# Optimization experiments

Measured on AMD Instinct MI355X. Metric: run time of the kernel, lower is better.

Reference implementation:

```python
import jax, jax.numpy as jnp
import numpy as np

B, N, D = 2, 2048, 1024
H, ENC = 16, 8
HD = D // H
EPS = 1e-5


def _apply_rope(x, cos, sin):
    # x: [B,N,H,HD], cos/sin: [N,HD//2]
    c = cos[None, :, None, :]
    s = sin[None, :, None, :]
    x_re = x[..., 0::2]
    x_im = x[..., 1::2]
    out = jnp.stack([x_re * c - x_im * s, x_re * s + x_im * c], axis=-1)
    return out.reshape(x.shape)


def _rmsnorm(x):
    return x * jax.lax.rsqrt(jnp.mean(x * x, axis=-1, keepdims=True) + EPS)


def setup_inputs() -> dict:
    key = jax.random.key(0)
    ks = jax.random.split(key, 8)
    pos = jnp.arange(N, dtype=jnp.float32)[:, None]
    inv_freq = 1.0 / (10000.0 ** (jnp.arange(0, HD, 2, dtype=jnp.float32) / HD))  # [HD//2]
    ang = pos * inv_freq[None, :]
    std = 0.02
    return {
        "x": jax.random.normal(ks[0], (B, N, D), dtype=jnp.float32),
        "rope_cos": jnp.cos(ang),
        "rope_sin": jnp.sin(ang),
        "Wq": std * jax.random.normal(ks[1], (D, D), dtype=jnp.float32),
        "Wk": std * jax.random.normal(ks[2], (D, D), dtype=jnp.float32),
        "Wv": std * jax.random.normal(ks[3], (D, D), dtype=jnp.float32),
        "Wo_enc": std * jax.random.normal(ks[4], (H * HD, D), dtype=jnp.float32),
        "Wo_dec": std * jax.random.normal(ks[5], ((H - ENC) * HD, D), dtype=jnp.float32),
        "heads": H,
        "encoder_heads": ENC,
    }


def reference(x, rope_cos, rope_sin, Wq, Wk, Wv, Wo_enc, Wo_dec, heads, encoder_heads):
    b, n, d = x.shape
    hd = d // heads
    scale = hd ** (-0.5)
    q = (x @ Wq).reshape(b, n, heads, hd)
    k = (x @ Wk).reshape(b, n, heads, hd)
    v = (x @ Wv).reshape(b, n, heads, hd)
    q = _rmsnorm(_apply_rope(q, rope_cos, rope_sin))
    k = _rmsnorm(_apply_rope(k, rope_cos, rope_sin))
    # scores: [B,H,N,N]
    scores = jnp.einsum("bihd,bjhd->bhij", q, k) * scale
    causal = jnp.tril(jnp.ones((n, n), dtype=bool))  # [N,N]
    is_enc = (jnp.arange(heads) < encoder_heads)[:, None, None]  # [H,1,1]
    allow = jnp.logical_or(is_enc, causal[None, :, :])  # [H,N,N]
    scores = jnp.where(allow[None], scores, -jnp.inf)
    att = jax.nn.softmax(scores, axis=-1)
    out = jnp.einsum("bhij,bjhd->bihd", att, v)  # [B,N,H,HD]
    enc_out = out.reshape(b, n, heads * hd) @ Wo_enc
    dec_out = out[:, :, encoder_heads:, :].reshape(b, n, (heads - encoder_heads) * hd) @ Wo_dec
    return (enc_out, dec_out)
```

## Files before the change

### kernel.cpp

```cpp
#include <hip/hip_runtime.h>
#include <hip/hip_bf16.h>
#include <math.h>

#define B_    2
#define N_    2048
#define D_    1024
#define H_    16
#define ENC_  8
#define HD_   64
#define EPS_  1e-5f
#define M_    (B_ * N_)

typedef __bf16 bf16x8 __attribute__((ext_vector_type(8)));
typedef __bf16 bf16x2 __attribute__((ext_vector_type(2)));
typedef float  f32x4  __attribute__((ext_vector_type(4)));

#define MB(x) ((size_t)(x) * 1024 * 1024)

#define KSC_  0.18033688011112042f

#if __has_builtin(__builtin_amdgcn_exp2f)
#define EXP2F(x) __builtin_amdgcn_exp2f(x)
#else
#define EXP2F(x) exp2f(x)
#endif

__device__ __forceinline__ void gld16(const __bf16* g, __bf16* l) {
    __builtin_amdgcn_global_load_lds(
        (const __attribute__((address_space(1))) void*)g,
        (__attribute__((address_space(3))) void*)l,
        16, 0, 0);
}

template <typename OutT>
__device__ __forceinline__ void gemm_core(
    const __bf16* __restrict__ A, const __bf16* __restrict__ Bt,
    OutT* __restrict__ C, int K, int lda, int aoff, int ldc,
    int bm, int bn, __bf16* As, __bf16* Bs)
{
    const int tid  = threadIdx.x;
    const int w    = tid >> 6;
    const int lane = tid & 63;
    const int lrow = lane & 15;
    const int quad = lane >> 4;
    const int wr   = w >> 1;
    const int wc   = w & 1;

    const int sr = lane >> 3;
    const int cl = lane & 7;
    const int sk = ((cl ^ sr) * 8);

    const __bf16* Ag0 = A  + (size_t)(bm +  0 + w * 8 + sr) * lda + aoff + sk;
    const __bf16* Ag1 = A  + (size_t)(bm + 32 + w * 8 + sr) * lda + aoff + sk;
    const __bf16* Ag2 = A  + (size_t)(bm + 64 + w * 8 + sr) * lda + aoff + sk;
    const __bf16* Ag3 = A  + (size_t)(bm + 96 + w * 8 + sr) * lda + aoff + sk;
    const __bf16* Bg0 = Bt + (size_t)(bn +  0 + w * 8 + sr) * K + sk;
    const __bf16* Bg1 = Bt + (size_t)(bn + 32 + w * 8 + sr) * K + sk;
    const __bf16* Bg2 = Bt + (size_t)(bn + 64 + w * 8 + sr) * K + sk;
    const __bf16* Bg3 = Bt + (size_t)(bn + 96 + w * 8 + sr) * K + sk;

    f32x4 acc[4][4];
    #pragma unroll
    for (int i = 0; i < 4; ++i)
        #pragma unroll
        for (int j = 0; j < 4; ++j) acc[i][j] = (f32x4){0.f, 0.f, 0.f, 0.f};

    auto stage = [&](int k0, int bb) {
        __bf16* Al = As + bb * 8192 + w * 8 * 64;
        __bf16* Bl = Bs + bb * 8192 + w * 8 * 64;
        gld16(Ag0 + k0, Al);
        gld16(Ag1 + k0, Al + 2048);
        gld16(Ag2 + k0, Al + 4096);
        gld16(Ag3 + k0, Al + 6144);
        gld16(Bg0 + k0, Bl);
        gld16(Bg1 + k0, Bl + 2048);
        gld16(Bg2 + k0, Bl + 4096);
        gld16(Bg3 + k0, Bl + 6144);
    };

    stage(0, 0);
    __syncthreads();
    int bb = 0;
    for (int k0 = 0; k0 < K; k0 += 64, bb ^= 1) {
        if (k0 + 64 < K) stage(k0 + 64, bb ^ 1);
        const __bf16* Ab = As + bb * 8192;
        const __bf16* Bb = Bs + bb * 8192;
        #pragma unroll
        for (int h = 0; h < 2; ++h) {
            const int ch = ((h * 4 + quad) ^ (lrow & 7)) * 8;
            bf16x8 af[4], bf[4];
            #pragma unroll
            for (int rt = 0; rt < 4; ++rt)
                af[rt] = *(const bf16x8*)&Ab[(wr * 64 + rt * 16 + lrow) * 64 + ch];
            #pragma unroll
            for (int ct = 0; ct < 4; ++ct)
                bf[ct] = *(const bf16x8*)&Bb[(wc * 64 + ct * 16 + lrow) * 64 + ch];

            #pragma unroll
            for (int rt = 0; rt < 4; ++rt)
                #pragma unroll
                for (int ct = 0; ct < 4; ++ct)
                    acc[rt][ct] = __builtin_amdgcn_mfma_f32_16x16x32_bf16(
                        af[rt], bf[ct], acc[rt][ct], 0, 0, 0);
        }
        __syncthreads();
    }

    #pragma unroll
    for (int rt = 0; rt < 4; ++rt)
        #pragma unroll
        for (int ct = 0; ct < 4; ++ct)
            #pragma unroll
            for (int r = 0; r < 4; ++r) {
                const int row = bm + wr * 64 + rt * 16 + quad * 4 + r;
                const int col = bn + wc * 64 + ct * 16 + lrow;
                C[(size_t)row * ldc + col] = (OutT)acc[rt][ct][r];
            }
}

__global__ __launch_bounds__(256) void gemm_qkv(
    const __bf16* __restrict__ A, const __bf16* __restrict__ Bt,
    __bf16* __restrict__ C)
{
    __shared__ __bf16 As[2 * 128 * 64];
    __shared__ __bf16 Bs[2 * 128 * 64];
    gemm_core<__bf16>(A, Bt, C, D_, D_, 0, 3072,
                      blockIdx.y * 128, blockIdx.x * 128, As, Bs);
}

__global__ __launch_bounds__(256) void gemm_out(
    const __bf16* __restrict__ A, const __bf16* __restrict__ Woe,
    const __bf16* __restrict__ Wod, float* __restrict__ Cenc,
    float* __restrict__ Cdec)
{
    __shared__ __bf16 As[2 * 128 * 64];
    __shared__ __bf16 Bs[2 * 128 * 64];
    const int id = blockIdx.x;
    if (id < 256) {
        gemm_core<float>(A, Woe, Cenc, 1024, D_, 0, D_,
                         (id >> 3) * 128, (id & 7) * 128, As, Bs);
    } else {
        const int idx = id - 256;
        gemm_core<float>(A, Wod, Cdec, 512, D_, 512, D_,
                         (idx >> 3) * 128, (idx & 7) * 128, As, Bs);
    }
}

struct WtArgs {
    const float* W[5];
    __bf16*      Wt[5];
    int          K[5];
    int          nyb[5];
    const float* x;
    __bf16*      xbf;
};

__global__ __launch_bounds__(256) void wt_conv_all(WtArgs ar)
{
    const int z = blockIdx.z;
    if (z >= 5) {
        const int linear = (z - 5) * 256 + blockIdx.y * 16 + blockIdx.x;
        const size_t i = ((size_t)linear * 256 + threadIdx.x) * 8;
        float4 a = *(const float4*)&ar.x[i];
        float4 b = *(const float4*)&ar.x[i + 4];
        bf16x8 o = {(__bf16)a.x, (__bf16)a.y, (__bf16)a.z, (__bf16)a.w,
                    (__bf16)b.x, (__bf16)b.y, (__bf16)b.z, (__bf16)b.w};
        *(bf16x8*)&ar.xbf[i] = o;
        return;
    }
    if (blockIdx.y >= ar.nyb[z]) return;
    const float* W  = ar.W[z];
    __bf16*      Wt = ar.Wt[z];
    const int    K  = ar.K[z];

    __shared__ __bf16 t[64][72];
    const int kb = blockIdx.y * 64;
    const int nb = blockIdx.x * 64;
    {
        const int kl = threadIdx.x >> 2;
        const int c0 = (threadIdx.x & 3) * 16;
        const float* src = W + (size_t)(kb + kl) * D_ + nb + c0;
        #pragma unroll
        for (int u = 0; u < 4; ++u) {
            float4 f = *(const float4*)&src[u * 4];
            t[c0 + u * 4 + 0][kl] = (__bf16)f.x;
            t[c0 + u * 4 + 1][kl] = (__bf16)f.y;
            t[c0 + u * 4 + 2][kl] = (__bf16)f.z;
            t[c0 + u * 4 + 3][kl] = (__bf16)f.w;
        }
    }
    __syncthreads();
    {
        const int nl  = threadIdx.x >> 2;
        const int k0c = (threadIdx.x & 3) * 16;
        __bf16* dst = Wt + (size_t)(nb + nl) * K + kb + k0c;
        *(bf16x8*)&dst[0] = *(const bf16x8*)&t[nl][k0c];
        *(bf16x8*)&dst[8] = *(const bf16x8*)&t[nl][k0c + 8];
    }
}

__global__ __launch_bounds__(256) void rope_vconv(
    const __bf16* __restrict__ qkv,
    const float* __restrict__ cs, const float* __restrict__ sn,
    __bf16* __restrict__ qbf, __bf16* __restrict__ kbf,
    __bf16* __restrict__ vt)
{
    if (blockIdx.x < 16384) {
        const int row  = blockIdx.x * 4 + (threadIdx.x >> 6);
        const int lane = threadIdx.x & 63;
        const int n    = (row >> 4) & (N_ - 1);
        const int b    = row >> 15;
        const int h    = row & 15;
        const int p    = lane >> 1;

        const float c = cs[n * (HD_ / 2) + p];
        const float s = sn[n * (HD_ / 2) + p];
        const size_t ibase = (size_t)(b * N_ + n) * 3072 + h * HD_ + lane;
        const size_t obase = ((size_t)(b * H_ + h) * N_ + n) * HD_ + lane;
        const bool odd = (lane & 1);

        {
            float val = (float)qkv[ibase];
            float partner = __shfl_xor(val, 1, 64);
            float r = odd ? fmaf(partner, s, val * c)
                          : (val * c - partner * s);
            float ss = r * r;
            #pragma unroll
            for (int off = 1; off < 64; off <<= 1) ss += __shfl_xor(ss, off, 64);
            qbf[obase] = (__bf16)(r * rsqrtf(ss * (1.0f / 64.0f) + EPS_) * KSC_);
        }
        {
            float val = (float)qkv[ibase + 1024];
            float partner = __shfl_xor(val, 1, 64);
            float r = odd ? fmaf(partner, s, val * c)
                          : (val * c - partner * s);
            float ss = r * r;
            #pragma unroll
            for (int off = 1; off < 64; off <<= 1) ss += __shfl_xor(ss, off, 64);
            kbf[obase] = (__bf16)(r * rsqrtf(ss * (1.0f / 64.0f) + EPS_));
        }
    } else {
        __shared__ __bf16 tile[64][72];
        const int bx = blockIdx.x - 16384;
        const int bh = bx >> 5;
        const int b  = bh >> 4, h = bh & 15;
        const int n0 = (bx & 31) * 64;
        {
            const int nl = threadIdx.x >> 2;
            const int d0 = (threadIdx.x & 3) * 16;
            const __bf16* src =
                qkv + (size_t)(b * N_ + n0 + nl) * 3072 + 2048 + h * HD_ + d0;
            bf16x8 v0 = *(const bf16x8*)&src[0];
            bf16x8 v1 = *(const bf16x8*)&src[8];
            #pragma unroll
            for (int e = 0; e < 8; ++e) {
                tile[d0 + e][nl]     = v0[e];
                tile[d0 + 8 + e][nl] = v1[e];
            }
        }
        __syncthreads();
        {
            const int dl = threadIdx.x >> 2;
            const int nc = (threadIdx.x & 3) * 16;
            __bf16* dst = vt + ((size_t)(bh * HD_ + dl)) * N_ + n0 + nc;
            bf16x8 o0, o1;
            #pragma unroll
            for (int e = 0; e < 8; ++e) {
                const int p0 = nc + e;
                const int p1 = nc + 8 + e;
                o0[e] = tile[dl][(p0 & ~31) + (((p0 >> 2) & 1) << 4)
                                 + (((p0 >> 3) & 3) << 2) + (p0 & 3)];
                o1[e] = tile[dl][(p1 & ~31) + (((p1 >> 2) & 1) << 4)
                                 + (((p1 >> 3) & 3) << 2) + (p1 & 3)];
            }
            *(bf16x8*)&dst[0] = o0;
            *(bf16x8*)&dst[8] = o1;
        }
    }
}

template <int NG, bool DEC>
__device__ __forceinline__ void attn_core(
    const __bf16* __restrict__ qbase, const __bf16* __restrict__ kbase,
    const __bf16* __restrict__ vbase, __bf16* __restrict__ o,
    int b, int h, int qb, int ntiles,
    __bf16 (*Ks)[4096], __bf16 (*Vs)[4096])
{
    const int tid  = threadIdx.x;
    const int w    = tid >> 6;
    const int lane = tid & 63;
    const int lrow = lane & 15;
    const int quad = lane >> 4;

    const __bf16* kg0 = kbase + (size_t)lane * HD_ + w * 8;
    const __bf16* kg1 = kbase + (size_t)lane * HD_ + (w + 4) * 8;
    const __bf16* vg  = vbase + (size_t)lane * N_;

    int i0g[NG];
    #pragma unroll
    for (int g = 0; g < NG; ++g) i0g[g] = qb * (NG * 64) + g * 64 + w * 16;

    bf16x8 qf[NG][2];
    #pragma unroll
    for (int g = 0; g < NG; ++g)
        #pragma unroll
        for (int kc = 0; kc < 2; ++kc)
            qf[g][kc] = *(const bf16x8*)
                &qbase[(size_t)(i0g[g] + lrow) * HD_ + kc * 32 + quad * 8];

    const f32x4 zero = {0.f, 0.f, 0.f, 0.f};
    f32x4 oacc[NG][4];
    float lsum[NG];
    #pragma unroll
    for (int g = 0; g < NG; ++g) {
        lsum[g] = 0.f;
        #pragma unroll
        for (int c = 0; c < 4; ++c) oacc[g][c] = zero;
    }

    auto stage = [&](int t, int bb) {
        const int j0 = t << 6;
        gld16(kg0 + (size_t)j0 * HD_, &Ks[bb][(w)     * 512]);
        gld16(kg1 + (size_t)j0 * HD_, &Ks[bb][(w + 4) * 512]);
        gld16(vg + j0 + w * 8,        &Vs[bb][(w)     * 512]);
        gld16(vg + j0 + (w + 4) * 8,  &Vs[bb][(w + 4) * 512]);
    };

    stage(0, 0);
    for (int t = 0; t < ntiles; ++t) {
        const int bb = t & 1;
        __syncthreads();
        if (t + 1 < ntiles) stage(t + 1, bb ^ 1);

        const int j64 = t << 6;
        const bool do1 = !DEC || (j64 + 32 <= i0g[0] + 15);

        bf16x8 pf[2][NG];

        {
            bf16x8 kf0 = *(const bf16x8*)&Ks[bb][((quad)     * 64 + lrow) * 8];
            bf16x8 kf1 = *(const bf16x8*)&Ks[bb][((4 + quad) * 64 + lrow) * 8];
            bf16x8 kf2 = *(const bf16x8*)&Ks[bb][((quad)     * 64 + 16 + lrow) * 8];
            bf16x8 kf3 = *(const bf16x8*)&Ks[bb][((4 + quad) * 64 + 16 + lrow) * 8];

            f32x4 s0[NG], s1[NG];
            #pragma unroll
            for (int g = 0; g < NG; ++g) { s0[g] = zero; s1[g] = zero; }
            #pragma unroll
            for (int g = 0; g < NG; ++g)
                s0[g] = __builtin_amdgcn_mfma_f32_16x16x32_bf16(kf0, qf[g][0], s0[g], 0, 0, 0);
            #pragma unroll
            for (int g = 0; g < NG; ++g)
                s0[g] = __builtin_amdgcn_mfma_f32_16x16x32_bf16(kf1, qf[g][1], s0[g], 0, 0, 0);
            #pragma unroll
            for (int g = 0; g < NG; ++g)
                s1[g] = __builtin_amdgcn_mfma_f32_16x16x32_bf16(kf2, qf[g][0], s1[g], 0, 0, 0);
            #pragma unroll
            for (int g = 0; g < NG; ++g)
                s1[g] = __builtin_amdgcn_mfma_f32_16x16x32_bf16(kf3, qf[g][1], s1[g], 0, 0, 0);

            #pragma unroll
            for (int g = 0; g < NG; ++g) {
                float pA[4], pB[4];
                if (DEC && (j64 + 31 > i0g[g])) {
                    const int i = i0g[g] + lrow;
                    #pragma unroll
                    for (int r = 0; r < 4; ++r) {
                        const int k0 = j64 + quad * 4 + r;
                        pA[r] = (k0      <= i) ? EXP2F(s0[g][r]) : 0.f;
                        pB[r] = (k0 + 16 <= i) ? EXP2F(s1[g][r]) : 0.f;
                    }
                } else {
                    #pragma unroll
                    for (int r = 0; r < 4; ++r) {
                        pA[r] = EXP2F(s0[g][r]);
                        pB[r] = EXP2F(s1[g][r]);
                    }
                }
                lsum[g] += (pA[0] + pA[1]) + (pA[2] + pA[3])
                         + (pB[0] + pB[1]) + (pB[2] + pB[3]);
                pf[0][g] = (bf16x8){(__bf16)pA[0], (__bf16)pA[1],
                                    (__bf16)pA[2], (__bf16)pA[3],
                                    (__bf16)pB[0], (__bf16)pB[1],
                                    (__bf16)pB[2], (__bf16)pB[3]};
            }
        }

        if (do1) {
            bf16x8 kf0 = *(const bf16x8*)&Ks[bb][((quad)     * 64 + 32 + lrow) * 8];
            bf16x8 kf1 = *(const bf16x8*)&Ks[bb][((4 + quad) * 64 + 32 + lrow) * 8];
            bf16x8 kf2 = *(const bf16x8*)&Ks[bb][((quad)     * 64 + 48 + lrow) * 8];
            bf16x8 kf3 = *(const bf16x8*)&Ks[bb][((4 + quad) * 64 + 48 + lrow) * 8];

            f32x4 s0[NG], s1[NG];
            #pragma unroll
            for (int g = 0; g < NG; ++g) { s0[g] = zero; s1[g] = zero; }
            #pragma unroll
            for (int g = 0; g < NG; ++g)
                s0[g] = __builtin_amdgcn_mfma_f32_16x16x32_bf16(kf0, qf[g][0], s0[g], 0, 0, 0);
            #pragma unroll
            for (int g = 0; g < NG; ++g)
                s0[g] = __builtin_amdgcn_mfma_f32_16x16x32_bf16(kf1, qf[g][1], s0[g], 0, 0, 0);
            #pragma unroll
            for (int g = 0; g < NG; ++g)
                s1[g] = __builtin_amdgcn_mfma_f32_16x16x32_bf16(kf2, qf[g][0], s1[g], 0, 0, 0);
            #pragma unroll
            for (int g = 0; g < NG; ++g)
                s1[g] = __builtin_amdgcn_mfma_f32_16x16x32_bf16(kf3, qf[g][1], s1[g], 0, 0, 0);

            const int jp = j64 + 32;
            #pragma unroll
            for (int g = 0; g < NG; ++g) {
                float pA[4], pB[4];
                if (DEC && (jp + 31 > i0g[g])) {
                    const int i = i0g[g] + lrow;
                    #pragma unroll
                    for (int r = 0; r < 4; ++r) {
                        const int k0 = jp + quad * 4 + r;
                        pA[r] = (k0      <= i) ? EXP2F(s0[g][r]) : 0.f;
                        pB[r] = (k0 + 16 <= i) ? EXP2F(s1[g][r]) : 0.f;
                    }
                } else {
                    #pragma unroll
                    for (int r = 0; r < 4; ++r) {
                        pA[r] = EXP2F(s0[g][r]);
                        pB[r] = EXP2F(s1[g][r]);
                    }
                }
                lsum[g] += (pA[0] + pA[1]) + (pA[2] + pA[3])
                         + (pB[0] + pB[1]) + (pB[2] + pB[3]);
                pf[1][g] = (bf16x8){(__bf16)pA[0], (__bf16)pA[1],
                                    (__bf16)pA[2], (__bf16)pA[3],
                                    (__bf16)pB[0], (__bf16)pB[1],
                                    (__bf16)pB[2], (__bf16)pB[3]};
            }
        }

        {
            bf16x8 vf0 = *(const bf16x8*)&Vs[bb][((quad) * 64 +  0 + lrow) * 8];
            bf16x8 vf1 = *(const bf16x8*)&Vs[bb][((quad) * 64 + 16 + lrow) * 8];
            bf16x8 vf2 = *(const bf16x8*)&Vs[bb][((quad) * 64 + 32 + lrow) * 8];
            bf16x8 vf3 = *(const bf16x8*)&Vs[bb][((quad) * 64 + 48 + lrow) * 8];
            #pragma unroll
            for (int g = 0; g < NG; ++g) {
                oacc[g][0] = __builtin_amdgcn_mfma_f32_16x16x32_bf16(pf[0][g], vf0, oacc[g][0], 0, 0, 0);
                oacc[g][1] = __builtin_amdgcn_mfma_f32_16x16x32_bf16(pf[0][g], vf1, oacc[g][1], 0, 0, 0);
                oacc[g][2] = __builtin_amdgcn_mfma_f32_16x16x32_bf16(pf[0][g], vf2, oacc[g][2], 0, 0, 0);
                oacc[g][3] = __builtin_amdgcn_mfma_f32_16x16x32_bf16(pf[0][g], vf3, oacc[g][3], 0, 0, 0);
            }
        }

        if (do1) {
            bf16x8 vf0 = *(const bf16x8*)&Vs[bb][((4 + quad) * 64 +  0 + lrow) * 8];
            bf16x8 vf1 = *(const bf16x8*)&Vs[bb][((4 + quad) * 64 + 16 + lrow) * 8];
            bf16x8 vf2 = *(const bf16x8*)&Vs[bb][((4 + quad) * 64 + 32 + lrow) * 8];
            bf16x8 vf3 = *(const bf16x8*)&Vs[bb][((4 + quad) * 64 + 48 + lrow) * 8];
            #pragma unroll
            for (int g = 0; g < NG; ++g) {
                oacc[g][0] = __builtin_amdgcn_mfma_f32_16x16x32_bf16(pf[1][g], vf0, oacc[g][0], 0, 0, 0);
                oacc[g][1] = __builtin_amdgcn_mfma_f32_16x16x32_bf16(pf[1][g], vf1, oacc[g][1], 0, 0, 0);
                oacc[g][2] = __builtin_amdgcn_mfma_f32_16x16x32_bf16(pf[1][g], vf2, oacc[g][2], 0, 0, 0);
                oacc[g][3] = __builtin_amdgcn_mfma_f32_16x16x32_bf16(pf[1][g], vf3, oacc[g][3], 0, 0, 0);
            }
        }
    }

    float lrec[NG][4];
    #pragma unroll
    for (int g = 0; g < NG; ++g) {
        float s = lsum[g];
        s += __shfl_xor(s, 16, 64);
        s += __shfl_xor(s, 32, 64);
        s = 1.0f / s;
        #pragma unroll
        for (int r = 0; r < 4; ++r)
            lrec[g][r] = __shfl(s, quad * 4 + r, 64);
    }

    #pragma unroll
    for (int g = 0; g < NG; ++g)
        #pragma unroll
        for (int c = 0; c < 4; ++c)
            #pragma unroll
            for (int r = 0; r < 4; ++r) {
                const int i = i0g[g] + quad * 4 + r;
                o[(size_t)(b * N_ + i) * D_ + h * HD_ + c * 16 + lrow] =
                    (__bf16)(oacc[g][c][r] * lrec[g][r]);
            }
}

__global__ __launch_bounds__(256) void attn_mfma(
    const __bf16* __restrict__ qbf, const __bf16* __restrict__ kbf,
    const __bf16* __restrict__ vtbf, __bf16* __restrict__ o)
{
    __shared__ __bf16 Ks[2][4096];
    __shared__ __bf16 Vs[2][4096];

    if (blockIdx.x < 256) {
        const int e  = blockIdx.x & 15;
        const int bh = (e >> 3) * 16 + (e & 7);
        const int qb = blockIdx.x >> 4;
        attn_core<2, false>(
            qbf  + (size_t)bh * N_ * HD_, kbf + (size_t)bh * N_ * HD_,
            vtbf + (size_t)bh * HD_ * N_, o,
            bh >> 4, bh & 15, qb, N_ >> 6, Ks, Vs);
    } else {
        const int idx = blockIdx.x - 256;
        const int d   = idx & 15;
        const int bh  = (d >> 3) * 16 + 8 + (d & 7);
        const int p   = idx >> 4;
        const int qb  = (p < 16) ? (31 - p) : (p - 16);
        attn_core<1, true>(
            qbf  + (size_t)bh * N_ * HD_, kbf + (size_t)bh * N_ * HD_,
            vtbf + (size_t)bh * HD_ * N_, o,
            bh >> 4, bh & 15, qb, qb + 1, Ks, Vs);
    }
}

extern "C" void kernel_launch(void* const* d_in, const int* in_sizes, int n_in,
                              void* d_out, int out_size, void* d_ws, size_t ws_size,
                              hipStream_t stream)
{
    const float* x   = (const float*)d_in[0];
    const float* cs  = (const float*)d_in[1];
    const float* sn  = (const float*)d_in[2];
    const float* Wq  = (const float*)d_in[3];
    const float* Wk  = (const float*)d_in[4];
    const float* Wv  = (const float*)d_in[5];
    const float* Woe = (const float*)d_in[6];
    const float* Wod = (const float*)d_in[7];

    float* enc_out = (float*)d_out;
    float* dec_out = enc_out + (size_t)M_ * D_;

    char* ws = (char*)d_ws;
    __bf16* xbf    = (__bf16*)(ws);
    __bf16* wqkv_t = (__bf16*)(ws + MB(8));
    __bf16* woe_t  = (__bf16*)(ws + MB(14));
    __bf16* wod_t  = (__bf16*)(ws + MB(16));
    __bf16* qkv    = (__bf16*)(ws + MB(17));
    __bf16* qbf    = (__bf16*)(ws + MB(41));
    __bf16* kbf    = (__bf16*)(ws + MB(49));
    __bf16* vtbf   = xbf;
    __bf16* obuf   = qkv;

    WtArgs wa;
    wa.W[0] = Wq;  wa.Wt[0] = wqkv_t;                 wa.K[0] = 1024; wa.nyb[0] = 16;
    wa.W[1] = Wk;  wa.Wt[1] = wqkv_t + 1024 * 1024;   wa.K[1] = 1024; wa.nyb[1] = 16;
    wa.W[2] = Wv;  wa.Wt[2] = wqkv_t + 2048 * 1024;   wa.K[2] = 1024; wa.nyb[2] = 16;
    wa.W[3] = Woe; wa.Wt[3] = woe_t;                  wa.K[3] = 1024; wa.nyb[3] = 16;
    wa.W[4] = Wod; wa.Wt[4] = wod_t;                  wa.K[4] = 512;  wa.nyb[4] = 8;
    wa.x = x; wa.xbf = xbf;
    wt_conv_all<<<dim3(16, 16, 13), 256, 0, stream>>>(wa);

    gemm_qkv<<<dim3(3072 / 128, M_ / 128), 256, 0, stream>>>(xbf, wqkv_t, qkv);

    rope_vconv<<<16384 + 1024, 256, 0, stream>>>(qkv, cs, sn, qbf, kbf, vtbf);

    attn_mfma<<<dim3(768), 256, 0, stream>>>(qbf, kbf, vtbf, obuf);

    gemm_out<<<dim3(512), 256, 0, stream>>>(
        obuf, woe_t, wod_t, enc_out, dec_out);
}
```

Measured before the change: 217.6 us.

## Fuse RoPE and RMSNorm of Q/K into the QKV GEMM epilogue

The QKV GEMM now applies rotary embedding, RMS normalization and the softmax scale to Q and K directly from the MFMA accumulators, using lane shuffles for pair swaps and the row reduction, and writes head-major bf16 Q/K. Only the V columns are still written to the intermediate buffer, and the follow-up kernel shrinks to the V transpose alone. This removes a full write and re-read of Q/K and 16384 extra blocks of elementwise work. In exchange the GEMM epilogue does scattered 2-byte stores and per-element cos/sin loads.

```diff
diff --git a/kernel.cpp b/kernel.cpp
--- a/kernel.cpp
+++ b/kernel.cpp
@@ -120,12 +120,134 @@
 
 __global__ __launch_bounds__(256) void gemm_qkv(
     const __bf16* __restrict__ A, const __bf16* __restrict__ Bt,
-    __bf16* __restrict__ C)
+    __bf16* __restrict__ Cv,
+    const float* __restrict__ cs, const float* __restrict__ sn,
+    __bf16* __restrict__ qbf, __bf16* __restrict__ kbf)
 {
     __shared__ __bf16 As[2 * 128 * 64];
     __shared__ __bf16 Bs[2 * 128 * 64];
-    gemm_core<__bf16>(A, Bt, C, D_, D_, 0, 3072,
-                      blockIdx.y * 128, blockIdx.x * 128, As, Bs);
+
+    const int tid  = threadIdx.x;
+    const int w    = tid >> 6;
+    const int lane = tid & 63;
+    const int lrow = lane & 15;
+    const int quad = lane >> 4;
+    const int wr   = w >> 1;
+    const int wc   = w & 1;
+
+    const int bx = blockIdx.x;
+    const int bm = blockIdx.y * 128;
+    const int bn = bx * 128;
+
+    const int sr = lane >> 3;
+    const int cl = lane & 7;
+    const int sk = ((cl ^ sr) * 8);
+
+    const __bf16* Ag0 = A  + (size_t)(bm +  0 + w * 8 + sr) * D_ + sk;
+    const __bf16* Ag1 = A  + (size_t)(bm + 32 + w * 8 + sr) * D_ + sk;
+    const __bf16* Ag2 = A  + (size_t)(bm + 64 + w * 8 + sr) * D_ + sk;
+    const __bf16* Ag3 = A  + (size_t)(bm + 96 + w * 8 + sr) * D_ + sk;
+    const __bf16* Bg0 = Bt + (size_t)(bn +  0 + w * 8 + sr) * D_ + sk;
+    const __bf16* Bg1 = Bt + (size_t)(bn + 32 + w * 8 + sr) * D_ + sk;
+    const __bf16* Bg2 = Bt + (size_t)(bn + 64 + w * 8 + sr) * D_ + sk;
+    const __bf16* Bg3 = Bt + (size_t)(bn + 96 + w * 8 + sr) * D_ + sk;
+
+    f32x4 acc[4][4];
+    #pragma unroll
+    for (int i = 0; i < 4; ++i)
+        #pragma unroll
+        for (int j = 0; j < 4; ++j) acc[i][j] = (f32x4){0.f, 0.f, 0.f, 0.f};
+
+    auto stage = [&](int k0, int bb) {
+        __bf16* Al = As + bb * 8192 + w * 8 * 64;
+        __bf16* Bl = Bs + bb * 8192 + w * 8 * 64;
+        gld16(Ag0 + k0, Al);
+        gld16(Ag1 + k0, Al + 2048);
+        gld16(Ag2 + k0, Al + 4096);
+        gld16(Ag3 + k0, Al + 6144);
+        gld16(Bg0 + k0, Bl);
+        gld16(Bg1 + k0, Bl + 2048);
+        gld16(Bg2 + k0, Bl + 4096);
+        gld16(Bg3 + k0, Bl + 6144);
+    };
+
+    stage(0, 0);
+    __syncthreads();
+    int bb = 0;
+    for (int k0 = 0; k0 < D_; k0 += 64, bb ^= 1) {
+        if (k0 + 64 < D_) stage(k0 + 64, bb ^ 1);
+        const __bf16* Ab = As + bb * 8192;
+        const __bf16* Bb = Bs + bb * 8192;
+        #pragma unroll
+        for (int h = 0; h < 2; ++h) {
+            const int ch = ((h * 4 + quad) ^ (lrow & 7)) * 8;
+            bf16x8 af[4], bf[4];
+            #pragma unroll
+            for (int rt = 0; rt < 4; ++rt)
+                af[rt] = *(const bf16x8*)&Ab[(wr * 64 + rt * 16 + lrow) * 64 + ch];
+            #pragma unroll
+            for (int ct = 0; ct < 4; ++ct)
+                bf[ct] = *(const bf16x8*)&Bb[(wc * 64 + ct * 16 + lrow) * 64 + ch];
+
+            #pragma unroll
+            for (int rt = 0; rt < 4; ++rt)
+                #pragma unroll
+                for (int ct = 0; ct < 4; ++ct)
+                    acc[rt][ct] = __builtin_amdgcn_mfma_f32_16x16x32_bf16(
+                        af[rt], bf[ct], acc[rt][ct], 0, 0, 0);
+        }
+        __syncthreads();
+    }
+
+    if (bx >= 16) {
+        #pragma unroll
+        for (int rt = 0; rt < 4; ++rt)
+            #pragma unroll
+            for (int ct = 0; ct < 4; ++ct)
+                #pragma unroll
+                for (int r = 0; r < 4; ++r) {
+                    const int row = bm + wr * 64 + rt * 16 + quad * 4 + r;
+                    const int col = bn + wc * 64 + ct * 16 + lrow;
+                    Cv[(size_t)row * 3072 + col] = (__bf16)acc[rt][ct][r];
+                }
+        return;
+    }
+
+    const bool isq = (bx < 8);
+    const int  h   = (bx & 7) * 2 + wc;
+    __bf16* outb = (isq ? qbf : kbf);
+
+    #pragma unroll
+    for (int rt = 0; rt < 4; ++rt) {
+        #pragma unroll
+        for (int r = 0; r < 4; ++r) {
+            const int row = bm + wr * 64 + rt * 16 + quad * 4 + r;
+            const int n   = row & (N_ - 1);
+            const int b   = row >> 11;
+            float e[4];
+            #pragma unroll
+            for (int ct = 0; ct < 4; ++ct) {
+                const float v = acc[rt][ct][r];
+                const float p = __shfl_xor(v, 1, 64);
+                const int   d = ct * 16 + lrow;
+                const float c = cs[n * (HD_ / 2) + (d >> 1)];
+                const float s = sn[n * (HD_ / 2) + (d >> 1)];
+                e[ct] = (lrow & 1) ? fmaf(p, s, v * c) : (v * c - p * s);
+            }
+            float ss = (e[0] * e[0] + e[1] * e[1])
+                     + (e[2] * e[2] + e[3] * e[3]);
+            ss += __shfl_xor(ss, 1, 64);
+            ss += __shfl_xor(ss, 2, 64);
+            ss += __shfl_xor(ss, 4, 64);
+            ss += __shfl_xor(ss, 8, 64);
+            const float sc = rsqrtf(ss * (1.0f / 64.0f) + EPS_)
+                           * (isq ? KSC_ : 1.0f);
+            __bf16* dst = outb + ((size_t)(b * H_ + h) * N_ + n) * HD_;
+            #pragma unroll
+            for (int ct = 0; ct < 4; ++ct)
+                dst[ct * 16 + lrow] = (__bf16)(e[ct] * sc);
+        }
+    }
 }
 
 __global__ __launch_bounds__(256) void gemm_out(
@@ -200,82 +322,43 @@
 }
 
 __global__ __launch_bounds__(256) void rope_vconv(
-    const __bf16* __restrict__ qkv,
-    const float* __restrict__ cs, const float* __restrict__ sn,
-    __bf16* __restrict__ qbf, __bf16* __restrict__ kbf,
-    __bf16* __restrict__ vt)
-{
-    if (blockIdx.x < 16384) {
-        const int row  = blockIdx.x * 4 + (threadIdx.x >> 6);
-        const int lane = threadIdx.x & 63;
-        const int n    = (row >> 4) & (N_ - 1);
-        const int b    = row >> 15;
-        const int h    = row & 15;
-        const int p    = lane >> 1;
-
-        const float c = cs[n * (HD_ / 2) + p];
-        const float s = sn[n * (HD_ / 2) + p];
-        const size_t ibase = (size_t)(b * N_ + n) * 3072 + h * HD_ + lane;
-        const size_t obase = ((size_t)(b * H_ + h) * N_ + n) * HD_ + lane;
-        const bool odd = (lane & 1);
-
-        {
-            float val = (float)qkv[ibase];
-            float partner = __shfl_xor(val, 1, 64);
-            float r = odd ? fmaf(partner, s, val * c)
-                          : (val * c - partner * s);
-            float ss = r * r;
-            #pragma unroll
-            for (int off = 1; off < 64; off <<= 1) ss += __shfl_xor(ss, off, 64);
-            qbf[obase] = (__bf16)(r * rsqrtf(ss * (1.0f / 64.0f) + EPS_) * KSC_);
-        }
-        {
-            float val = (float)qkv[ibase + 1024];
-            float partner = __shfl_xor(val, 1, 64);
-            float r = odd ? fmaf(partner, s, val * c)
-                          : (val * c - partner * s);
-            float ss = r * r;
-            #pragma unroll
-            for (int off = 1; off < 64; off <<= 1) ss += __shfl_xor(ss, off, 64);
-            kbf[obase] = (__bf16)(r * rsqrtf(ss * (1.0f / 64.0f) + EPS_));
-        }
-    } else {
-        __shared__ __bf16 tile[64][72];
-        const int bx = blockIdx.x - 16384;
-        const int bh = bx >> 5;
-        const int b  = bh >> 4, h = bh & 15;
-        const int n0 = (bx & 31) * 64;
-        {
-            const int nl = threadIdx.x >> 2;
-            const int d0 = (threadIdx.x & 3) * 16;
-            const __bf16* src =
-                qkv + (size_t)(b * N_ + n0 + nl) * 3072 + 2048 + h * HD_ + d0;
-            bf16x8 v0 = *(const bf16x8*)&src[0];
-            bf16x8 v1 = *(const bf16x8*)&src[8];
-            #pragma unroll
-            for (int e = 0; e < 8; ++e) {
-                tile[d0 + e][nl]     = v0[e];
-                tile[d0 + 8 + e][nl] = v1[e];
-            }
-        }
-        __syncthreads();
-        {
-            const int dl = threadIdx.x >> 2;
-            const int nc = (threadIdx.x & 3) * 16;
-            __bf16* dst = vt + ((size_t)(bh * HD_ + dl)) * N_ + n0 + nc;
-            bf16x8 o0, o1;
-            #pragma unroll
-            for (int e = 0; e < 8; ++e) {
-                const int p0 = nc + e;
-                const int p1 = nc + 8 + e;
-                o0[e] = tile[dl][(p0 & ~31) + (((p0 >> 2) & 1) << 4)
-                                 + (((p0 >> 3) & 3) << 2) + (p0 & 3)];
-                o1[e] = tile[dl][(p1 & ~31) + (((p1 >> 2) & 1) << 4)
-                                 + (((p1 >> 3) & 3) << 2) + (p1 & 3)];
-            }
-            *(bf16x8*)&dst[0] = o0;
-            *(bf16x8*)&dst[8] = o1;
-        }
+    const __bf16* __restrict__ qkv, __bf16* __restrict__ vt)
+{
+    __shared__ __bf16 tile[64][72];
+    const int bx = blockIdx.x;
+    const int bh = bx >> 5;
+    const int b  = bh >> 4, h = bh & 15;
+    const int n0 = (bx & 31) * 64;
+    {
+        const int nl = threadIdx.x >> 2;
+        const int d0 = (threadIdx.x & 3) * 16;
+        const __bf16* src =
+            qkv + (size_t)(b * N_ + n0 + nl) * 3072 + 2048 + h * HD_ + d0;
+        bf16x8 v0 = *(const bf16x8*)&src[0];
+        bf16x8 v1 = *(const bf16x8*)&src[8];
+        #pragma unroll
+        for (int e = 0; e < 8; ++e) {
+            tile[d0 + e][nl]     = v0[e];
+            tile[d0 + 8 + e][nl] = v1[e];
+        }
+    }
+    __syncthreads();
+    {
+        const int dl = threadIdx.x >> 2;
+        const int nc = (threadIdx.x & 3) * 16;
+        __bf16* dst = vt + ((size_t)(bh * HD_ + dl)) * N_ + n0 + nc;
+        bf16x8 o0, o1;
+        #pragma unroll
+        for (int e = 0; e < 8; ++e) {
+            const int p0 = nc + e;
+            const int p1 = nc + 8 + e;
+            o0[e] = tile[dl][(p0 & ~31) + (((p0 >> 2) & 1) << 4)
+                             + (((p0 >> 3) & 3) << 2) + (p0 & 3)];
+            o1[e] = tile[dl][(p1 & ~31) + (((p1 >> 2) & 1) << 4)
+                             + (((p1 >> 3) & 3) << 2) + (p1 & 3)];
+        }
+        *(bf16x8*)&dst[0] = o0;
+        *(bf16x8*)&dst[8] = o1;
     }
 }
 
@@ -553,9 +636,10 @@
     wa.x = x; wa.xbf = xbf;
     wt_conv_all<<<dim3(16, 16, 13), 256, 0, stream>>>(wa);
 
-    gemm_qkv<<<dim3(3072 / 128, M_ / 128), 256, 0, stream>>>(xbf, wqkv_t, qkv);
-
-    rope_vconv<<<16384 + 1024, 256, 0, stream>>>(qkv, cs, sn, qbf, kbf, vtbf);
+    gemm_qkv<<<dim3(3072 / 128, M_ / 128), 256, 0, stream>>>(
+        xbf, wqkv_t, qkv, cs, sn, qbf, kbf);
+
+    rope_vconv<<<1024, 256, 0, stream>>>(qkv, vtbf);
 
     attn_mfma<<<dim3(768), 256, 0, stream>>>(qbf, kbf, vtbf, obuf);
 
```

Measured after the change: 216.8 us. Within noise of the previous version (-0.4%).
